# Kernel optimization log

Measured on AMD Instinct MI355X. Metric: run time of the kernel, lower is better.

Reference implementation:

```python
import jax, jax.numpy as jnp
import numpy as np

N_NODES = 50000
N_EDGES = 512000
D = 128          # node_state_dim
H = 256          # edge hidden / message dim = 2*D (GRU input size)


def _edge_mlp(x, W1, b1, W2, b2):
    # Linear -> ReLU -> Linear, matching nn.Sequential built in build_model
    h = jax.nn.relu(x @ W1.T + b1)
    return h @ W2.T + b2


def _prop_once(node_states, f_idx, t_idx, W1, b1, W2, b2):
    # gather endpoints, concat, edge MLP, scatter-add into destination nodes
    edge_in = jnp.concatenate([node_states[f_idx], node_states[t_idx]], axis=-1)  # [E, 2D]
    msgs = _edge_mlp(edge_in, W1, b1, W2, b2)                                     # [E, H]
    return jax.ops.segment_sum(msgs, t_idx, num_segments=N_NODES)                 # [N, H]


def _gru_cell(x, h, W_ih, W_hh, b_ih, b_hh):
    # PyTorch GRU cell convention
    gi = x @ W_ih.T + b_ih   # [N, 3D]
    gh = h @ W_hh.T + b_hh   # [N, 3D]
    ir, iz, inn = jnp.split(gi, 3, axis=-1)
    hr, hz, hn = jnp.split(gh, 3, axis=-1)
    r = jax.nn.sigmoid(ir + hr)
    z = jax.nn.sigmoid(iz + hz)
    n = jnp.tanh(inn + r * hn)
    return (1.0 - z) * n + z * h


def setup_inputs() -> dict:
    key = jax.random.key(0)
    ks = jax.random.split(key, 16)
    s = 0.1  # edge_net_init_scale-ish small init
    inp = {
        "node_states": jax.random.normal(ks[0], (N_NODES, D), dtype=jnp.float32),
        "from_idx": jax.random.randint(ks[1], (N_EDGES,), 0, N_NODES),
        "to_idx": jax.random.randint(ks[2], (N_EDGES,), 0, N_NODES),
        # forward message net: Linear(2D->H), Linear(H->H)
        "Wf1": jax.random.normal(ks[3], (H, 2 * D), dtype=jnp.float32) * s,
        "bf1": jnp.zeros((H,), jnp.float32),
        "Wf2": jax.random.normal(ks[4], (H, H), dtype=jnp.float32) * s,
        "bf2": jnp.zeros((H,), jnp.float32),
        # reverse message net (separate params)
        "Wr1": jax.random.normal(ks[5], (H, 2 * D), dtype=jnp.float32) * s,
        "br1": jnp.zeros((H,), jnp.float32),
        "Wr2": jax.random.normal(ks[6], (H, H), dtype=jnp.float32) * s,
        "br2": jnp.zeros((H,), jnp.float32),
        # GRU(input=2D, hidden=D) params, torch layout
        "W_ih": jax.random.normal(ks[7], (3 * D, 2 * D), dtype=jnp.float32) * 0.05,
        "W_hh": jax.random.normal(ks[8], (3 * D, D), dtype=jnp.float32) * 0.05,
        "b_ih": jnp.zeros((3 * D,), jnp.float32),
        "b_hh": jnp.zeros((3 * D,), jnp.float32),
    }
    return inp


def reference(node_states, from_idx, to_idx, Wf1, bf1, Wf2, bf2,
              Wr1, br1, Wr2, br2, W_ih, W_hh, b_ih, b_hh):
    agg = _prop_once(node_states, from_idx, to_idx, Wf1, bf1, Wf2, bf2)
    agg = agg + _prop_once(node_states, to_idx, from_idx, Wr1, br1, Wr2, br2)
    return _gru_cell(agg, node_states, W_ih, W_hh, b_ih, b_hh)  # [N, D]
```

## Files before the change

kernel.cpp:

```cpp
#include <hip/hip_runtime.h>
#include <stdint.h>


#define NN 50000
#define NE 512000
#define SCAN_N (2 * NN)
#define SCAN_BLOCKS ((SCAN_N + 1023) / 1024)

typedef unsigned short u16;
typedef unsigned int u32;
using h2  = __attribute__((ext_vector_type(2))) _Float16;
using h4  = __attribute__((ext_vector_type(4))) _Float16;
using h8  = __attribute__((ext_vector_type(8))) _Float16;
using f4v = __attribute__((ext_vector_type(4))) float;

__device__ __forceinline__ float h2f(u16 u) {
  _Float16 h; __builtin_memcpy(&h, &u, 2); return (float)h;
}
__device__ __forceinline__ u16 f2h(float f) {
  _Float16 h = (_Float16)f; u16 u; __builtin_memcpy(&u, &h, 2); return u;
}

__global__ __launch_bounds__(256) void k_prep(
    const float* __restrict__ Wf1, const float* __restrict__ bf1,
    const float* __restrict__ Wr1, const float* __restrict__ br1,
    const float* __restrict__ W_ih, const float* __restrict__ Wf2,
    const float* __restrict__ Wr2, const float* __restrict__ W_hh,
    const float* __restrict__ bf2, const float* __restrict__ br2,
    const float* __restrict__ ns,
    u16* __restrict__ Wc16, float* __restrict__ biascat,
    u16* __restrict__ G16, u16* __restrict__ Wh16,
    float* __restrict__ vf, float* __restrict__ vr,
    u16* __restrict__ nsf) {
  const int b = blockIdx.x, tid = threadIdx.x;
  if (b < 512) {
    int c = b * 2 + (tid >> 7);
    int k = tid & 127;
    const float* src;
    if (c < 256)      src = Wf1 + (size_t)c * 256;
    else if (c < 512) src = Wr1 + (size_t)(c - 256) * 256 + 128;
    else if (c < 768) src = Wf1 + (size_t)(c - 512) * 256 + 128;
    else              src = Wr1 + (size_t)(c - 768) * 256;
    float v = src[k];
    int nt = c >> 4, kt = k >> 5, g = (k & 31) >> 3, j = k & 7;
    int lane = (c & 15) + g * 16;
    Wc16[((size_t)nt * 4 + kt) * 512 + lane * 8 + j] = f2h(v);
    if (k == 0) biascat[c] = (c < 256) ? bf1[c] : ((c >= 768) ? br1[c - 768] : 0.f);
  } else if (b < 1280) {
    int bb = b - 512;
    int c = bb % 384, w = bb / 384;
    const float* W2 = w ? Wr2 : Wf2;
    int k = tid;
    float acc = 0.f;
    for (int o = 0; o < 256; ++o)
      acc = fmaf(W_ih[(size_t)c * 256 + o], W2[(size_t)o * 256 + k], acc);
    int kg = w * 256 + k;
    int nt = c >> 4, kt = kg >> 5, g = (kg & 31) >> 3, j = kg & 7;
    int lane = (c & 15) + g * 16;
    G16[((size_t)nt * 16 + kt) * 512 + lane * 8 + j] = f2h(acc);
  } else if (b < 1472) {
    int c = (b - 1280) * 2 + (tid >> 7);
    int k = tid & 127;
    float v = W_hh[(size_t)c * 128 + k];
    int nt = c >> 4, kt = k >> 5, g = (k & 31) >> 3, j = k & 7;
    int lane = (c & 15) + g * 16;
    Wh16[((size_t)nt * 4 + kt) * 512 + lane * 8 + j] = f2h(v);
  } else if (b < 1474) {
    int c = (b - 1472) * 256 + tid;
    if (c < 384) {
      float a = 0.f, bb = 0.f;
      for (int o = 0; o < 256; ++o) {
        float w = W_ih[(size_t)c * 256 + o];
        a = fmaf(w, bf2[o], a);
        bb = fmaf(w, br2[o], bb);
      }
      vf[c] = a; vr[c] = bb;
    }
  } else {
    int t = (b - 1474) * 256 + tid;
    int n = t >> 4, kk8 = t & 15;
    float4 v0 = *(const float4*)(ns + (size_t)n * 128 + kk8 * 8);
    float4 v1 = *(const float4*)(ns + (size_t)n * 128 + kk8 * 8 + 4);
    u16 hv[8] = {f2h(v0.x), f2h(v0.y), f2h(v0.z), f2h(v0.w),
                 f2h(v1.x), f2h(v1.y), f2h(v1.z), f2h(v1.w)};
    int mt = n >> 4, r = n & 15, kt = kk8 >> 2, g = kk8 & 3;
    int lane = r + g * 16;
    *(uint4*)(nsf + ((size_t)mt * 4 + kt) * 512 + lane * 8) = *(const uint4*)hv;
  }
}

__global__ void k_hist(const int* __restrict__ from, const int* __restrict__ to,
                       int* __restrict__ cnt) {
  int e = blockIdx.x * 256 + threadIdx.x;
  if (e < NE) {
    atomicAdd(cnt + to[e], 1);
    atomicAdd(cnt + NN + from[e], 1);
  }
}

__global__ __launch_bounds__(256) void k_scanA(const int* __restrict__ cnt,
                                               int* __restrict__ bsum) {
  __shared__ int part[256];
  int b = blockIdx.x, tid = threadIdx.x;
  int idx = b * 1024 + tid * 4;
  int s = 0;
  if (idx + 3 < SCAN_N) {
    int4 v = *(const int4*)(cnt + idx);
    s = v.x + v.y + v.z + v.w;
  } else {
    for (int q = 0; q < 4; ++q)
      if (idx + q < SCAN_N) s += cnt[idx + q];
  }
  part[tid] = s;
  __syncthreads();
  for (int d = 128; d > 0; d >>= 1) {
    if (tid < d) part[tid] += part[tid + d];
    __syncthreads();
  }
  if (tid == 0) bsum[b] = part[0];
}

__global__ __launch_bounds__(256) void k_scanC(const int* __restrict__ cnt,
                                               const int* __restrict__ bsum,
                                               int* __restrict__ off,
                                               int* __restrict__ cur) {
  __shared__ int part[256];
  __shared__ int bs[SCAN_BLOCKS];
  int b = blockIdx.x, tid = threadIdx.x;
  if (tid < SCAN_BLOCKS) bs[tid] = bsum[tid];
  int idx = b * 1024 + tid * 4;
  int c[4] = {0, 0, 0, 0};
  if (idx + 3 < SCAN_N) {
    int4 v = *(const int4*)(cnt + idx);
    c[0] = v.x; c[1] = v.y; c[2] = v.z; c[3] = v.w;
  } else {
    for (int q = 0; q < 4; ++q)
      if (idx + q < SCAN_N) c[q] = cnt[idx + q];
  }
  int s = c[0] + c[1] + c[2] + c[3];
  part[tid] = s;
  __syncthreads();
  for (int d = 1; d < 256; d <<= 1) {
    int x = (tid >= d) ? part[tid - d] : 0;
    __syncthreads();
    part[tid] += x;
    __syncthreads();
  }
  int pre = 0;
  for (int j = 0; j < b; ++j) pre += bs[j];
  int run = pre + ((tid > 0) ? part[tid - 1] : 0);
#pragma unroll
  for (int q = 0; q < 4; ++q) {
    if (idx + q < SCAN_N) {
      off[idx + q] = run;
      cur[idx + q] = run;
      run += c[q];
    }
  }
  if (b == 0 && tid == 0) off[SCAN_N] = 2 * NE;
}

__global__ void k_fill(const int* __restrict__ from, const int* __restrict__ to,
                       int* __restrict__ cur, int* __restrict__ nbr) {
  int e = blockIdx.x * 256 + threadIdx.x;
  if (e < NE) {
    int f = from[e], t = to[e];
    nbr[atomicAdd(cur + t, 1)] = f;
    nbr[atomicAdd(cur + NN + f, 1)] = t;
  }
}

__global__ __launch_bounds__(256) void k_proj(const u16* __restrict__ nsf,
                                              const u16* __restrict__ Wc16,
                                              const float* __restrict__ biascat,
                                              u16* __restrict__ Tin,
                                              u16* __restrict__ Tnode,
                                              u16* __restrict__ Tout) {
  const int w = threadIdx.x >> 6, lane = threadIdx.x & 63;
  const int mt0 = blockIdx.x * 4;
  const int nt0 = blockIdx.y * 16 + w * 4;
  const h8 hzv = {(_Float16)0.f, (_Float16)0.f, (_Float16)0.f, (_Float16)0.f,
                  (_Float16)0.f, (_Float16)0.f, (_Float16)0.f, (_Float16)0.f};
  f4v acc[4][4];
#pragma unroll
  for (int m = 0; m < 4; ++m)
#pragma unroll
    for (int n = 0; n < 4; ++n) acc[m][n] = (f4v){0.f, 0.f, 0.f, 0.f};

#pragma unroll
  for (int kt = 0; kt < 4; ++kt) {
    h8 a[4], b[4];
#pragma unroll
    for (int m = 0; m < 4; ++m) {
      int mt = mt0 + m;
      a[m] = (mt < 3125) ? *(const h8*)(nsf + ((size_t)mt * 4 + kt) * 512 + lane * 8) : hzv;
    }
#pragma unroll
    for (int n = 0; n < 4; ++n)
      b[n] = *(const h8*)(Wc16 + ((size_t)(nt0 + n) * 4 + kt) * 512 + lane * 8);
#pragma unroll
    for (int m = 0; m < 4; ++m)
#pragma unroll
      for (int n = 0; n < 4; ++n)
        acc[m][n] = __builtin_amdgcn_mfma_f32_16x16x32_f16(a[m], b[n], acc[m][n], 0, 0, 0);
  }

  const int c0 = lane & 15, rB = (lane >> 4) * 4;
#pragma unroll
  for (int n = 0; n < 4; ++n) {
    const int ntg = nt0 + n;
    u16* dst;
    size_t stride;
    int col;
    if (ntg < 16)      { dst = Tin;   stride = 256; col = ntg * 16 + c0; }
    else if (ntg < 48) { dst = Tnode; stride = 512; col = (ntg - 16) * 16 + c0; }
    else               { dst = Tout;  stride = 256; col = (ntg - 48) * 16 + c0; }
    float bias = biascat[ntg * 16 + c0];
#pragma unroll
    for (int m = 0; m < 4; ++m) {
      int mt = mt0 + m;
      if (mt >= 3125) continue;
#pragma unroll
      for (int reg = 0; reg < 4; ++reg) {
        int row = mt * 16 + rB + reg;
        dst[(size_t)row * stride + col] = f2h(acc[m][n][reg] + bias);
      }
    }
  }
}

__global__ __launch_bounds__(256) void k_gather(const u16* __restrict__ Tin,
                                                const u16* __restrict__ Tnode,
                                                const u16* __restrict__ Tout,
                                                const int* __restrict__ nbr,
                                                const int* __restrict__ off,
                                                u16* __restrict__ Sf) {
  const int lane = threadIdx.x & 63;
  const int gid = blockIdx.x * 4 + (threadIdx.x >> 6);
  const int dir = (gid >= NN) ? 1 : 0;
  const int n = gid - dir * NN;
  const int mt = n >> 4, r = n & 15;
  const int g = (lane & 7) >> 1, j0 = (lane & 1) * 4;
  const int laneF = r + g * 16;

  const u16* gtab = dir ? Tout : Tin;
  const int invofs = dir ? 0 : 256;
  const h2 z2 = {(_Float16)0.f, (_Float16)0.f};
  h4 invv = __builtin_nontemporal_load(
      (const h4*)(Tnode + (size_t)n * 512 + invofs + lane * 4));
  h2 inv01 = {invv[0], invv[1]};
  h2 inv23 = {invv[2], invv[3]};
  const int s = off[dir * NN + n];
  const int e = off[dir * NN + n + 1];
  float a0 = 0.f, a1 = 0.f, a2 = 0.f, a3 = 0.f;

#define LOADF(q_, kbase_) \
  (*(const h4*)(gtab + (size_t)__builtin_amdgcn_readlane(nb, (kbase_) + (q_)) * 256 + lane * 4))
#define CONSUME(wvq_)                                           \
  {                                                             \
    h2 t01 = {(wvq_)[0], (wvq_)[1]};                            \
    h2 t23 = {(wvq_)[2], (wvq_)[3]};                            \
    t01 = __builtin_elementwise_max(t01 + inv01, z2);           \
    t23 = __builtin_elementwise_max(t23 + inv23, z2);           \
    a0 += (float)t01[0]; a1 += (float)t01[1];                   \
    a2 += (float)t23[0]; a3 += (float)t23[1];                   \
  }

  for (int i = s; i < e; i += 64) {
    int nb = (i + lane < e) ? __builtin_nontemporal_load(nbr + i + lane) : 0;
    int cnt = min(64, e - i);
    int k = 0;
    for (; k + 7 < cnt; k += 8) {
      h4 w0 = LOADF(0, k), w1 = LOADF(1, k), w2 = LOADF(2, k), w3 = LOADF(3, k);
      h4 w4 = LOADF(4, k), w5 = LOADF(5, k), w6 = LOADF(6, k), w7 = LOADF(7, k);
      CONSUME(w0) CONSUME(w1) CONSUME(w2) CONSUME(w3)
      CONSUME(w4) CONSUME(w5) CONSUME(w6) CONSUME(w7)
    }
    if (k + 3 < cnt) {
      h4 w0 = LOADF(0, k), w1 = LOADF(1, k), w2 = LOADF(2, k), w3 = LOADF(3, k);
      CONSUME(w0) CONSUME(w1) CONSUME(w2) CONSUME(w3)
      k += 4;
    }
    for (; k < cnt; ++k) {
      h4 w0 = LOADF(0, k);
      CONSUME(w0)
    }
  }
#undef LOADF
#undef CONSUME

  int kt = dir * 8 + (lane >> 3);
  u16 hv[4] = {f2h(a0), f2h(a1), f2h(a2), f2h(a3)};
  *(ushort4*)(Sf + ((size_t)mt * 16 + kt) * 512 + laneF * 8 + j0) = *(const ushort4*)hv;
}

__global__ __launch_bounds__(256) void k_gru(const u16* __restrict__ Sf,
                                             const u16* __restrict__ nsf,
                                             const u16* __restrict__ G16,
                                             const u16* __restrict__ Wh16,
                                             const float* __restrict__ ns,
                                             const float* __restrict__ b_ih,
                                             const float* __restrict__ b_hh,
                                             const float* __restrict__ vf,
                                             const float* __restrict__ vr,
                                             const int* __restrict__ off,
                                             float* __restrict__ out) {
  const int w = threadIdx.x >> 6, lane = threadIdx.x & 63;
  const int mt0 = (blockIdx.x >> 1) * 2, half = blockIdx.x & 1;
  const int base = half * 4 + w;
  const bool has1 = (mt0 + 1) < 3125;
  const h8 hz = {(_Float16)0.f, (_Float16)0.f, (_Float16)0.f, (_Float16)0.f,
                 (_Float16)0.f, (_Float16)0.f, (_Float16)0.f, (_Float16)0.f};

  f4v gh[2][3], gi[2][3];
#pragma unroll
  for (int m = 0; m < 2; ++m)
#pragma unroll
    for (int g = 0; g < 3; ++g) {
      gh[m][g] = (f4v){0.f, 0.f, 0.f, 0.f};
      gi[m][g] = (f4v){0.f, 0.f, 0.f, 0.f};
    }

#pragma unroll
  for (int kt = 0; kt < 4; ++kt) {
    h8 a0 = *(const h8*)(nsf + ((size_t)mt0 * 4 + kt) * 512 + lane * 8);
    h8 a1 = has1 ? *(const h8*)(nsf + ((size_t)(mt0 + 1) * 4 + kt) * 512 + lane * 8) : hz;
#pragma unroll
    for (int g = 0; g < 3; ++g) {
      h8 b = *(const h8*)(Wh16 + ((size_t)(base + 8 * g) * 4 + kt) * 512 + lane * 8);
      gh[0][g] = __builtin_amdgcn_mfma_f32_16x16x32_f16(a0, b, gh[0][g], 0, 0, 0);
      gh[1][g] = __builtin_amdgcn_mfma_f32_16x16x32_f16(a1, b, gh[1][g], 0, 0, 0);
    }
  }

#pragma unroll
  for (int kt = 0; kt < 16; ++kt) {
    h8 a0 = *(const h8*)(Sf + ((size_t)mt0 * 16 + kt) * 512 + lane * 8);
    h8 a1 = has1 ? *(const h8*)(Sf + ((size_t)(mt0 + 1) * 16 + kt) * 512 + lane * 8) : hz;
#pragma unroll
    for (int g = 0; g < 3; ++g) {
      h8 b = *(const h8*)(G16 + ((size_t)(base + 8 * g) * 16 + kt) * 512 + lane * 8);
      gi[0][g] = __builtin_amdgcn_mfma_f32_16x16x32_f16(a0, b, gi[0][g], 0, 0, 0);
      gi[1][g] = __builtin_amdgcn_mfma_f32_16x16x32_f16(a1, b, gi[1][g], 0, 0, 0);
    }
  }

  const int c0 = lane & 15, rB = (lane >> 4) * 4;
  const int d = base * 16 + c0;
  const float vf0 = vf[d], vf1 = vf[128 + d], vf2 = vf[256 + d];
  const float vr0 = vr[d], vr1 = vr[128 + d], vr2 = vr[256 + d];
  const float bi0 = b_ih[d], bi1 = b_ih[128 + d], bi2 = b_ih[256 + d];
  const float bh0 = b_hh[d], bh1 = b_hh[128 + d], bh2 = b_hh[256 + d];
#pragma unroll
  for (int m = 0; m < 2; ++m) {
    if (m == 1 && !has1) continue;
    const int mt = mt0 + m;
#pragma unroll
    for (int reg = 0; reg < 4; ++reg) {
      int row = mt * 16 + rB + reg;
      float idg = (float)(off[row + 1] - off[row]);
      float odg = (float)(off[NN + row + 1] - off[NN + row]);
      float gr = gi[m][0][reg] + idg * vf0 + odg * vr0 + bi0;
      float gz = gi[m][1][reg] + idg * vf1 + odg * vr1 + bi1;
      float gn = gi[m][2][reg] + idg * vf2 + odg * vr2 + bi2;
      float hr = gh[m][0][reg] + bh0;
      float hzv = gh[m][1][reg] + bh1;
      float hn = gh[m][2][reg] + bh2;
      float rg = 1.f / (1.f + __expf(-(gr + hr)));
      float zg = 1.f / (1.f + __expf(-(gz + hzv)));
      float ng = tanhf(gn + rg * hn);
      float h = ns[(size_t)row * 128 + d];
      out[(size_t)row * 128 + d] = (1.f - zg) * ng + zg * h;
    }
  }
}

extern "C" void kernel_launch(void* const* d_in, const int* in_sizes, int n_in,
                              void* d_out, int out_size, void* d_ws, size_t ws_size,
                              hipStream_t stream) {
  const float* ns   = (const float*)d_in[0];
  const int* from   = (const int*)d_in[1];
  const int* to     = (const int*)d_in[2];
  const float* Wf1  = (const float*)d_in[3];
  const float* bf1  = (const float*)d_in[4];
  const float* Wf2  = (const float*)d_in[5];
  const float* bf2  = (const float*)d_in[6];
  const float* Wr1  = (const float*)d_in[7];
  const float* br1  = (const float*)d_in[8];
  const float* Wr2  = (const float*)d_in[9];
  const float* br2  = (const float*)d_in[10];
  const float* W_ih = (const float*)d_in[11];
  const float* W_hh = (const float*)d_in[12];
  const float* b_ih = (const float*)d_in[13];
  const float* b_hh = (const float*)d_in[14];
  float* out = (float*)d_out;

  char* w = (char*)d_ws;
  u16*   Wc16    = (u16*)(w + 0);
  float* biascat = (float*)(w + 262144);
  u16*   G16     = (u16*)(w + 266240);
  u16*   Wh16    = (u16*)(w + 659456);
  float* vf      = (float*)(w + 757760);
  float* vr      = (float*)(w + 759296);
  int*   cnt     = (int*)(w + 760832);
  int*   off     = (int*)(w + 1160960);
  int*   cur     = (int*)(w + 1561088);
  int*   bsum    = (int*)(w + 1961216);
  int*   nbr     = (int*)(w + 1961728);
  u16*   nsf     = (u16*)(w + 6057728);
  u16*   Tin     = (u16*)(w + 18857728);
  u16*   Tout    = (u16*)(w + 44457728);
  u16*   Tnode   = (u16*)(w + 70057728);
  u16*   Sf      = (u16*)(w + 121257728);

  hipMemsetAsync(cnt, 0, 400000, stream);

  k_prep<<<4599, 256, 0, stream>>>(Wf1, bf1, Wr1, br1, W_ih, Wf2, Wr2, W_hh,
                                   bf2, br2, ns, Wc16, biascat, G16, Wh16, vf, vr, nsf);

  k_hist<<<(NE + 255) / 256, 256, 0, stream>>>(from, to, cnt);
  k_scanA<<<SCAN_BLOCKS, 256, 0, stream>>>(cnt, bsum);
  k_scanC<<<SCAN_BLOCKS, 256, 0, stream>>>(cnt, bsum, off, cur);
  k_fill<<<(NE + 255) / 256, 256, 0, stream>>>(from, to, cur, nbr);

  k_proj<<<dim3(782, 4), 256, 0, stream>>>(nsf, Wc16, biascat, Tin, Tnode, Tout);
  k_gather<<<25000, 256, 0, stream>>>(Tin, Tnode, Tout, nbr, off, Sf);
  k_gru<<<3126, 256, 0, stream>>>(Sf, nsf, G16, Wh16, ns, b_ih, b_hh, vf, vr, off, out);
}
```

Before: 346.1 us.

## Fuse neighbor gather into GRU kernel via LDS and merge histogram into prep

The gather and GRU kernels are merged into one 512-thread kernel. Each block gathers the aggregated messages for two 16-row tiles, both directions, into shared memory, then runs the MFMA GRU directly from LDS. This removes the global round trip of the Sf buffer and one launch. The edge histogram also moves into extra k_prep blocks so it needs no separate launch. In exchange there are fewer blocks (1563), 8 gather tasks per wave done serially, and a block-wide barrier that may lower occupancy and latency hiding in the gather phase.

After: 343.4 us. Within noise of the previous version (-0.8%).

```diff
diff --git a/kernel.cpp b/kernel.cpp
--- a/kernel.cpp
+++ b/kernel.cpp
@@ -28,10 +28,11 @@
     const float* __restrict__ Wr2, const float* __restrict__ W_hh,
     const float* __restrict__ bf2, const float* __restrict__ br2,
     const float* __restrict__ ns,
+    const int* __restrict__ from, const int* __restrict__ to,
     u16* __restrict__ Wc16, float* __restrict__ biascat,
     u16* __restrict__ G16, u16* __restrict__ Wh16,
     float* __restrict__ vf, float* __restrict__ vr,
-    u16* __restrict__ nsf) {
+    u16* __restrict__ nsf, int* __restrict__ cnt) {
   const int b = blockIdx.x, tid = threadIdx.x;
   if (b < 512) {
     int c = b * 2 + (tid >> 7);
@@ -76,7 +77,7 @@
       }
       vf[c] = a; vr[c] = bb;
     }
-  } else {
+  } else if (b < 4599) {
     int t = (b - 1474) * 256 + tid;
     int n = t >> 4, kk8 = t & 15;
     float4 v0 = *(const float4*)(ns + (size_t)n * 128 + kk8 * 8);
@@ -86,15 +87,12 @@
     int mt = n >> 4, r = n & 15, kt = kk8 >> 2, g = kk8 & 3;
     int lane = r + g * 16;
     *(uint4*)(nsf + ((size_t)mt * 4 + kt) * 512 + lane * 8) = *(const uint4*)hv;
-  }
-}
-
-__global__ void k_hist(const int* __restrict__ from, const int* __restrict__ to,
-                       int* __restrict__ cnt) {
-  int e = blockIdx.x * 256 + threadIdx.x;
-  if (e < NE) {
-    atomicAdd(cnt + to[e], 1);
-    atomicAdd(cnt + NN + from[e], 1);
+  } else {
+    int e = (b - 4599) * 256 + tid;
+    if (e < NE) {
+      atomicAdd(cnt + to[e], 1);
+      atomicAdd(cnt + NN + from[e], 1);
+    }
   }
 }
 
@@ -229,31 +227,27 @@
   }
 }
 
-__global__ __launch_bounds__(256) void k_gather(const u16* __restrict__ Tin,
-                                                const u16* __restrict__ Tnode,
-                                                const u16* __restrict__ Tout,
-                                                const int* __restrict__ nbr,
-                                                const int* __restrict__ off,
-                                                u16* __restrict__ Sf) {
-  const int lane = threadIdx.x & 63;
-  const int gid = blockIdx.x * 4 + (threadIdx.x >> 6);
-  const int dir = (gid >= NN) ? 1 : 0;
-  const int n = gid - dir * NN;
-  const int mt = n >> 4, r = n & 15;
+__global__ __launch_bounds__(512) void k_fused(const u16* __restrict__ Tin,
+                                               const u16* __restrict__ Tnode,
+                                               const u16* __restrict__ Tout,
+                                               const int* __restrict__ nbr,
+                                               const int* __restrict__ off,
+                                               const u16* __restrict__ nsf,
+                                               const u16* __restrict__ G16,
+                                               const u16* __restrict__ Wh16,
+                                               const float* __restrict__ ns,
+                                               const float* __restrict__ b_ih,
+                                               const float* __restrict__ b_hh,
+                                               const float* __restrict__ vf,
+                                               const float* __restrict__ vr,
+                                               float* __restrict__ out) {
+  __shared__ u16 sfl[2 * 16 * 512];
+  const int wid = threadIdx.x >> 6, lane = threadIdx.x & 63;
+  const int mt0 = blockIdx.x * 2;
+  const bool has1 = (mt0 + 1) < 3125;
+  const h2 z2 = {(_Float16)0.f, (_Float16)0.f};
+
   const int g = (lane & 7) >> 1, j0 = (lane & 1) * 4;
-  const int laneF = r + g * 16;
-
-  const u16* gtab = dir ? Tout : Tin;
-  const int invofs = dir ? 0 : 256;
-  const h2 z2 = {(_Float16)0.f, (_Float16)0.f};
-  h4 invv = __builtin_nontemporal_load(
-      (const h4*)(Tnode + (size_t)n * 512 + invofs + lane * 4));
-  h2 inv01 = {invv[0], invv[1]};
-  h2 inv23 = {invv[2], invv[3]};
-  const int s = off[dir * NN + n];
-  const int e = off[dir * NN + n + 1];
-  float a0 = 0.f, a1 = 0.f, a2 = 0.f, a3 = 0.f;
-
 #define LOADF(q_, kbase_) \
   (*(const h4*)(gtab + (size_t)__builtin_amdgcn_readlane(nb, (kbase_) + (q_)) * 256 + lane * 4))
 #define CONSUME(wvq_)                                           \
@@ -265,60 +259,60 @@
     a0 += (float)t01[0]; a1 += (float)t01[1];                   \
     a2 += (float)t23[0]; a3 += (float)t23[1];                   \
   }
-
-  for (int i = s; i < e; i += 64) {
-    int nb = (i + lane < e) ? __builtin_nontemporal_load(nbr + i + lane) : 0;
-    int cnt = min(64, e - i);
-    int k = 0;
-    for (; k + 7 < cnt; k += 8) {
-      h4 w0 = LOADF(0, k), w1 = LOADF(1, k), w2 = LOADF(2, k), w3 = LOADF(3, k);
-      h4 w4 = LOADF(4, k), w5 = LOADF(5, k), w6 = LOADF(6, k), w7 = LOADF(7, k);
-      CONSUME(w0) CONSUME(w1) CONSUME(w2) CONSUME(w3)
-      CONSUME(w4) CONSUME(w5) CONSUME(w6) CONSUME(w7)
-    }
-    if (k + 3 < cnt) {
-      h4 w0 = LOADF(0, k), w1 = LOADF(1, k), w2 = LOADF(2, k), w3 = LOADF(3, k);
-      CONSUME(w0) CONSUME(w1) CONSUME(w2) CONSUME(w3)
-      k += 4;
-    }
-    for (; k < cnt; ++k) {
-      h4 w0 = LOADF(0, k);
-      CONSUME(w0)
-    }
+  for (int t = 0; t < 8; ++t) {
+    const int task = wid * 8 + t;
+    const int nn = task >> 1, dir = task & 1;
+    const int n = mt0 * 16 + nn;
+    if (n >= NN) continue;
+    const u16* gtab = dir ? Tout : Tin;
+    const int invofs = dir ? 0 : 256;
+    h4 invv = __builtin_nontemporal_load(
+        (const h4*)(Tnode + (size_t)n * 512 + invofs + lane * 4));
+    h2 inv01 = {invv[0], invv[1]};
+    h2 inv23 = {invv[2], invv[3]};
+    const int s = off[dir * NN + n];
+    const int e = off[dir * NN + n + 1];
+    float a0 = 0.f, a1 = 0.f, a2 = 0.f, a3 = 0.f;
+    for (int i = s; i < e; i += 64) {
+      int nb = (i + lane < e) ? __builtin_nontemporal_load(nbr + i + lane) : 0;
+      int cnt = min(64, e - i);
+      int k = 0;
+      for (; k + 7 < cnt; k += 8) {
+        h4 w0 = LOADF(0, k), w1 = LOADF(1, k), w2 = LOADF(2, k), w3 = LOADF(3, k);
+        h4 w4 = LOADF(4, k), w5 = LOADF(5, k), w6 = LOADF(6, k), w7 = LOADF(7, k);
+        CONSUME(w0) CONSUME(w1) CONSUME(w2) CONSUME(w3)
+        CONSUME(w4) CONSUME(w5) CONSUME(w6) CONSUME(w7)
+      }
+      if (k + 3 < cnt) {
+        h4 w0 = LOADF(0, k), w1 = LOADF(1, k), w2 = LOADF(2, k), w3 = LOADF(3, k);
+        CONSUME(w0) CONSUME(w1) CONSUME(w2) CONSUME(w3)
+        k += 4;
+      }
+      for (; k < cnt; ++k) {
+        h4 w0 = LOADF(0, k);
+        CONSUME(w0)
+      }
+    }
+    const int m = nn >> 4, r = nn & 15;
+    const int kt = dir * 8 + (lane >> 3);
+    const int laneF = r + g * 16;
+    u16 hv[4] = {f2h(a0), f2h(a1), f2h(a2), f2h(a3)};
+    *(ushort4*)(sfl + ((m * 16 + kt) * 512) + laneF * 8 + j0) = *(const ushort4*)hv;
   }
 #undef LOADF
 #undef CONSUME
-
-  int kt = dir * 8 + (lane >> 3);
-  u16 hv[4] = {f2h(a0), f2h(a1), f2h(a2), f2h(a3)};
-  *(ushort4*)(Sf + ((size_t)mt * 16 + kt) * 512 + laneF * 8 + j0) = *(const ushort4*)hv;
-}
-
-__global__ __launch_bounds__(256) void k_gru(const u16* __restrict__ Sf,
-                                             const u16* __restrict__ nsf,
-                                             const u16* __restrict__ G16,
-                                             const u16* __restrict__ Wh16,
-                                             const float* __restrict__ ns,
-                                             const float* __restrict__ b_ih,
-                                             const float* __restrict__ b_hh,
-                                             const float* __restrict__ vf,
-                                             const float* __restrict__ vr,
-                                             const int* __restrict__ off,
-                                             float* __restrict__ out) {
-  const int w = threadIdx.x >> 6, lane = threadIdx.x & 63;
-  const int mt0 = (blockIdx.x >> 1) * 2, half = blockIdx.x & 1;
-  const int base = half * 4 + w;
-  const bool has1 = (mt0 + 1) < 3125;
+  __syncthreads();
+
+  const int base = wid;
   const h8 hz = {(_Float16)0.f, (_Float16)0.f, (_Float16)0.f, (_Float16)0.f,
                  (_Float16)0.f, (_Float16)0.f, (_Float16)0.f, (_Float16)0.f};
-
   f4v gh[2][3], gi[2][3];
 #pragma unroll
   for (int m = 0; m < 2; ++m)
 #pragma unroll
-    for (int g = 0; g < 3; ++g) {
-      gh[m][g] = (f4v){0.f, 0.f, 0.f, 0.f};
-      gi[m][g] = (f4v){0.f, 0.f, 0.f, 0.f};
+    for (int gg = 0; gg < 3; ++gg) {
+      gh[m][gg] = (f4v){0.f, 0.f, 0.f, 0.f};
+      gi[m][gg] = (f4v){0.f, 0.f, 0.f, 0.f};
     }
 
 #pragma unroll
@@ -326,22 +320,22 @@
     h8 a0 = *(const h8*)(nsf + ((size_t)mt0 * 4 + kt) * 512 + lane * 8);
     h8 a1 = has1 ? *(const h8*)(nsf + ((size_t)(mt0 + 1) * 4 + kt) * 512 + lane * 8) : hz;
 #pragma unroll
-    for (int g = 0; g < 3; ++g) {
-      h8 b = *(const h8*)(Wh16 + ((size_t)(base + 8 * g) * 4 + kt) * 512 + lane * 8);
-      gh[0][g] = __builtin_amdgcn_mfma_f32_16x16x32_f16(a0, b, gh[0][g], 0, 0, 0);
-      gh[1][g] = __builtin_amdgcn_mfma_f32_16x16x32_f16(a1, b, gh[1][g], 0, 0, 0);
+    for (int gg = 0; gg < 3; ++gg) {
+      h8 b = *(const h8*)(Wh16 + ((size_t)(base + 8 * gg) * 4 + kt) * 512 + lane * 8);
+      gh[0][gg] = __builtin_amdgcn_mfma_f32_16x16x32_f16(a0, b, gh[0][gg], 0, 0, 0);
+      gh[1][gg] = __builtin_amdgcn_mfma_f32_16x16x32_f16(a1, b, gh[1][gg], 0, 0, 0);
     }
   }
 
 #pragma unroll
   for (int kt = 0; kt < 16; ++kt) {
-    h8 a0 = *(const h8*)(Sf + ((size_t)mt0 * 16 + kt) * 512 + lane * 8);
-    h8 a1 = has1 ? *(const h8*)(Sf + ((size_t)(mt0 + 1) * 16 + kt) * 512 + lane * 8) : hz;
-#pragma unroll
-    for (int g = 0; g < 3; ++g) {
-      h8 b = *(const h8*)(G16 + ((size_t)(base + 8 * g) * 16 + kt) * 512 + lane * 8);
-      gi[0][g] = __builtin_amdgcn_mfma_f32_16x16x32_f16(a0, b, gi[0][g], 0, 0, 0);
-      gi[1][g] = __builtin_amdgcn_mfma_f32_16x16x32_f16(a1, b, gi[1][g], 0, 0, 0);
+    h8 a0 = *(const h8*)(sfl + (0 * 16 + kt) * 512 + lane * 8);
+    h8 a1 = has1 ? *(const h8*)(sfl + (1 * 16 + kt) * 512 + lane * 8) : hz;
+#pragma unroll
+    for (int gg = 0; gg < 3; ++gg) {
+      h8 b = *(const h8*)(G16 + ((size_t)(base + 8 * gg) * 16 + kt) * 512 + lane * 8);
+      gi[0][gg] = __builtin_amdgcn_mfma_f32_16x16x32_f16(a0, b, gi[0][gg], 0, 0, 0);
+      gi[1][gg] = __builtin_amdgcn_mfma_f32_16x16x32_f16(a1, b, gi[1][gg], 0, 0, 0);
     }
   }
 
@@ -411,19 +405,18 @@
   u16*   Tin     = (u16*)(w + 18857728);
   u16*   Tout    = (u16*)(w + 44457728);
   u16*   Tnode   = (u16*)(w + 70057728);
-  u16*   Sf      = (u16*)(w + 121257728);
 
   hipMemsetAsync(cnt, 0, 400000, stream);
 
-  k_prep<<<4599, 256, 0, stream>>>(Wf1, bf1, Wr1, br1, W_ih, Wf2, Wr2, W_hh,
-                                   bf2, br2, ns, Wc16, biascat, G16, Wh16, vf, vr, nsf);
-
-  k_hist<<<(NE + 255) / 256, 256, 0, stream>>>(from, to, cnt);
+  k_prep<<<6599, 256, 0, stream>>>(Wf1, bf1, Wr1, br1, W_ih, Wf2, Wr2, W_hh,
+                                   bf2, br2, ns, from, to, Wc16, biascat, G16,
+                                   Wh16, vf, vr, nsf, cnt);
+
   k_scanA<<<SCAN_BLOCKS, 256, 0, stream>>>(cnt, bsum);
   k_scanC<<<SCAN_BLOCKS, 256, 0, stream>>>(cnt, bsum, off, cur);
   k_fill<<<(NE + 255) / 256, 256, 0, stream>>>(from, to, cur, nbr);
 
   k_proj<<<dim3(782, 4), 256, 0, stream>>>(nsf, Wc16, biascat, Tin, Tnode, Tout);
-  k_gather<<<25000, 256, 0, stream>>>(Tin, Tnode, Tout, nbr, off, Sf);
-  k_gru<<<3126, 256, 0, stream>>>(Sf, nsf, G16, Wh16, ns, b_ih, b_hh, vf, vr, off, out);
-}
+  k_fused<<<1563, 512, 0, stream>>>(Tin, Tnode, Tout, nbr, off, nsf, G16, Wh16,
+                                    ns, b_ih, b_hh, vf, vr, out);
+}
```
